# Performance work log

Hardware: AMD Instinct MI355X
Metric: run time of the kernel (lower is better)

Reference implementation:

```python
import jax, jax.numpy as jnp
import numpy as np

# Workspace layout (static slice bounds, per init_kwargs)
SS, SE = 0, 512        # spoke
HPS, HPE = 512, 768    # hub private
HSS, HSE = 768, 1024   # hub shared
TS, TE = 1024, 1088    # tag
HS, HE = 512, 1024     # full hub (priv + shared) for the read path

B, T, D_STATE, D_MODEL, D_LATENT = 8, 4096, 1088, 1024, 128


def setup_inputs() -> dict:
    key = jax.random.key(0)
    ks = jax.random.split(key, 10)
    scale = 0.02  # typical init scale for learned projections
    return {
        "S": jax.random.normal(ks[0], (B, T, D_STATE), jnp.float32),
        "w_spoke": jax.random.normal(ks[1], (B, T, SE - SS), jnp.float32),
        "w_hub_priv": jax.random.normal(ks[2], (B, T, HPE - HPS), jnp.float32),
        "w_hub_shared": jax.random.normal(ks[3], (B, T, HSE - HSS), jnp.float32),
        "tag": jax.random.normal(ks[4], (B, T, TE - TS), jnp.float32),
        "W_read": jax.random.normal(ks[5], (D_MODEL, D_STATE), jnp.float32) * scale,
        "cache": jnp.zeros((B, T, D_LATENT), jnp.float32),
        "latent": jax.random.normal(ks[6], (B, T, D_LATENT), jnp.float32),
        "Wk": jax.random.normal(ks[7], (D_MODEL, D_LATENT), jnp.float32) * scale,
        "Wv": jax.random.normal(ks[8], (D_MODEL, D_LATENT), jnp.float32) * scale,
    }


def reference(S, w_spoke, w_hub_priv, w_hub_shared, tag, W_read, cache, latent, Wk, Wv):
    # --- fused_workspace_write: four independent slice-adds into S ---
    S = S.at[:, :, SS:SE].add(w_spoke)
    S = S.at[:, :, HPS:HPE].add(w_hub_priv)
    S = S.at[:, :, HSS:HSE].add(w_hub_shared)
    S = S.at[:, :, TS:TE].add(tag)

    # --- fused_workspace_read: concat(spoke, hub, tag) then F.linear(., W_read) ---
    readable = jnp.concatenate(
        [S[:, :, SS:SE], S[:, :, HS:HE], S[:, :, TS:TE]], axis=-1
    )  # (B, T, D_STATE)
    out = jnp.einsum("btr,dr->btd", readable, W_read)  # (B, T, D_MODEL)

    # --- CWTLatentCache.update: overwrite latents at start_position=0 ---
    cache = jax.lax.dynamic_update_slice(cache, latent, (0, 0, 0))

    # --- K/V reconstruction from compressed latents via up-projections ---
    k = jnp.einsum("btl,dl->btd", cache, Wk)  # (B, T, D_MODEL)
    v = jnp.einsum("btl,dl->btd", cache, Wv)  # (B, T, D_MODEL)
    return (out, k, v)
```

## Files before the change

### kernel.cpp

```cpp
#include <hip/hip_runtime.h>

typedef __attribute__((ext_vector_type(8))) _Float16 half8;
typedef __attribute__((ext_vector_type(2))) __fp16 half2r;
typedef __attribute__((ext_vector_type(4))) float f32x4;

#define AS1 __attribute__((address_space(1)))
#define AS3 __attribute__((address_space(3)))

union H2U { half2r h; unsigned int u; };
union Frag { half8 v; unsigned long long d[2]; };

__device__ __forceinline__ unsigned int pk(float a, float b) {
    H2U x; x.h = __builtin_amdgcn_cvt_pkrtz(a, b); return x.u;
}

__device__ __forceinline__ void gload_lds16(const void* g, void* l) {
    __builtin_amdgcn_global_load_lds((const AS1 unsigned int*)g,
                                     (AS3 unsigned int*)l, 16, 0, 0);
}

#define W1_ROWB 2176
#define WS2_OFF 2228224
#define W2_ROWB 256
#define A_ROWB  2176

__device__ __forceinline__ void pick_w(int ks, const float* wsp, const float* whp,
                                       const float* whs, const float* wtg,
                                       const float*& wbase, int& wstr, int& wko) {
    if (ks < 8)       { wbase = wsp; wstr = 512; wko = ks * 64; }
    else if (ks < 12) { wbase = whp; wstr = 256; wko = ks * 64 - 512; }
    else if (ks < 16) { wbase = whs; wstr = 256; wko = ks * 64 - 768; }
    else              { wbase = wtg; wstr = 64;  wko = 0; }
}

__global__ __launch_bounds__(256) void prep_w(const float* __restrict__ Wr,
                                              const float* __restrict__ Wk,
                                              const float* __restrict__ Wv,
                                              char* __restrict__ ws) {
    int id = blockIdx.x * 256 + threadIdx.x;
    if (id < 272 * 1024) {
        int n = id / 272;
        int k = (id % 272) * 4;
        f32x4 w = *(const f32x4*)(Wr + (size_t)n * 1088 + k);
        uint2 q; q.x = pk(w.x, w.y); q.y = pk(w.z, w.w);
        size_t off = (size_t)n * W1_ROWB + ((k >> 6) << 7)
                   + (((k & 63) << 1) ^ ((n & 7) << 4));
        *(uint2*)(ws + off) = q;
    } else {
        int j = id - 272 * 1024;
        int r = j >> 5;
        int k = (j & 31) << 2;
        const float* src = (r < 1024) ? (Wk + (size_t)r * 128 + k)
                                      : (Wv + (size_t)(r - 1024) * 128 + k);
        f32x4 w = *(const f32x4*)src;
        uint2 q; q.x = pk(w.x, w.y); q.y = pk(w.z, w.w);
        size_t off = WS2_OFF + (size_t)r * W2_ROWB + ((k >> 6) << 7)
                   + (((k & 63) << 1) ^ ((r & 7) << 4));
        *(uint2*)(ws + off) = q;
    }
}

__global__ __launch_bounds__(256)
void fuse_a(const float* __restrict__ S, const float* __restrict__ wsp,
            const float* __restrict__ whp, const float* __restrict__ whs,
            const float* __restrict__ wtg, char* __restrict__ a16) {
    int u = blockIdx.x * 256 + threadIdx.x;
    int row = u / 272;
    int rem = u % 272;
    int ks = rem >> 4;
    int k4 = (rem & 15) << 2;

    const float* wbase; int wstr, wko;
    pick_w(ks, wsp, whp, whs, wtg, wbase, wstr, wko);

    f32x4 s4 = *(const f32x4*)(S + (size_t)row * 1088 + ks * 64 + k4);
    f32x4 w4 = *(const f32x4*)(wbase + (size_t)row * wstr + wko + k4);
    uint2 q; q.x = pk(s4.x + w4.x, s4.y + w4.y);
             q.y = pk(s4.z + w4.z, s4.w + w4.w);
    size_t off = (size_t)row * A_ROWB + (ks << 7)
               + (((k4) << 1) ^ ((row & 7) << 4));
    *(uint2*)(a16 + off) = q;
}

__global__ __launch_bounds__(256, 2)
void gemm_read(const char* __restrict__ wsA, const char* __restrict__ wws,
               float* __restrict__ out) {
    __shared__ char lds[65536];

    int bid = blockIdx.x;
    int wg   = (bid & 7) * 256 + (bid >> 3);
    int mblk = wg >> 3, nblk = wg & 7;
    int m0 = mblk << 7, n0 = nblk << 7;

    int tid = threadIdx.x;
    int lane = tid & 63, wid = tid >> 6;
    int wm = (wid >> 1) << 6, wn = (wid & 1) << 6;
    int lp = lane & 15, lg = lane >> 4;

    f32x4 acc[4][4] = {};

#define STAGE_T(KS, DL, BASE, ROWB, R0) do {                              \
        const char* grow = (BASE) + (size_t)(R0) * (ROWB) + (KS) * 128;   \
        _Pragma("unroll")                                                 \
        for (int c = 0; c < 4; ++c) {                                     \
            int s = c * 4096 + wid * 1024 + lane * 16;                    \
            int rr = s >> 7, cb = s & 127;                                \
            gload_lds16(grow + (size_t)rr * (ROWB) + cb,                  \
                        (DL) + c * 4096 + wid * 1024);                    \
        }                                                                 \
    } while (0)

#define COMPUTE(AL, BL) do {                                              \
        _Pragma("unroll")                                                 \
        for (int b = 0; b < 2; ++b) {                                     \
            Frag af[4], bf[4];                                            \
            _Pragma("unroll")                                             \
            for (int f = 0; f < 4; ++f) {                                 \
                int ra = wm + f * 16 + lp;  int xa = (ra & 7) << 4;       \
                af[f].d[0] = *(const unsigned long long*)((AL) + (ra << 7) + ((b * 64 + lg * 8) ^ xa));      \
                af[f].d[1] = *(const unsigned long long*)((AL) + (ra << 7) + ((b * 64 + 32 + lg * 8) ^ xa)); \
                int rb = wn + f * 16 + lp;  int xb = (rb & 7) << 4;       \
                bf[f].d[0] = *(const unsigned long long*)((BL) + (rb << 7) + ((b * 64 + lg * 8) ^ xb));      \
                bf[f].d[1] = *(const unsigned long long*)((BL) + (rb << 7) + ((b * 64 + 32 + lg * 8) ^ xb)); \
            }                                                             \
            _Pragma("unroll")                                             \
            for (int i = 0; i < 4; ++i)                                   \
                _Pragma("unroll")                                         \
                for (int j = 0; j < 4; ++j)                               \
                    acc[i][j] = __builtin_amdgcn_mfma_f32_16x16x32_f16(af[i].v, bf[j].v, acc[i][j], 0, 0, 0); \
        }                                                                 \
    } while (0)

    STAGE_T(0, lds,         wsA, A_ROWB,  m0);
    STAGE_T(0, lds + 32768, wws, W1_ROWB, n0);
    __syncthreads();

    for (int ks = 0; ks < 17; ++ks) {
        int co = (ks & 1) ? 16384 : 0;
        int no = co ^ 16384;
        if (ks < 16) {
            STAGE_T(ks + 1, lds + no,         wsA, A_ROWB,  m0);
            STAGE_T(ks + 1, lds + 32768 + no, wws, W1_ROWB, n0);
        }
        COMPUTE(lds + co, lds + 32768 + co);
        __syncthreads();
    }

    #pragma unroll
    for (int i = 0; i < 4; ++i)
        #pragma unroll
        for (int j = 0; j < 4; ++j) {
            int row = m0 + wm + i * 16 + (lg << 2);
            int col = n0 + wn + j * 16 + lp;
            float* p = out + (size_t)row * 1024 + col;
            #pragma unroll
            for (int r = 0; r < 4; ++r) p[(size_t)r * 1024] = acc[i][j][r];
        }
#undef STAGE_T
#undef COMPUTE
}

__global__ __launch_bounds__(256, 2)
void gemm_kv(const float* __restrict__ lat, const char* __restrict__ ws2,
             float* __restrict__ outk, float* __restrict__ outv) {
    __shared__ char lds[32768];
    char* Al = lds;
    char* Bl = lds + 16384;

    int bid = blockIdx.x;
    int wg   = (bid & 7) * 512 + (bid >> 3);
    int mblk = wg >> 4, nb = wg & 15;
    int m0 = mblk << 7;
    int nrow0 = nb << 7;
    float* out = (nb < 8) ? outk : outv;
    int n0 = (nb & 7) << 7;

    int tid = threadIdx.x;
    int lane = tid & 63, wid = tid >> 6;
    int wm = (wid >> 1) << 6, wn = (wid & 1) << 6;
    int lp = lane & 15, lg = lane >> 4;

    f32x4 acc[4][4] = {};

    for (int ks = 0; ks < 2; ++ks) {
        __syncthreads();
        {
            const char* wrow = ws2 + (size_t)nrow0 * W2_ROWB + ks * 128;
            #pragma unroll
            for (int c = 0; c < 4; ++c) {
                int s = c * 4096 + wid * 1024 + lane * 16;
                int n = s >> 7, cb = s & 127;
                gload_lds16(wrow + (size_t)n * W2_ROWB + cb,
                            Bl + c * 4096 + wid * 1024);
            }
        }
        #pragma unroll
        for (int i = 0; i < 8; ++i) {
            int u = i * 256 + tid;
            int row = u >> 4;
            int k4 = (u & 15) << 2;
            f32x4 s4 = *(const f32x4*)(lat + (size_t)(m0 + row) * 128 + ks * 64 + k4);
            uint2 q; q.x = pk(s4.x, s4.y); q.y = pk(s4.z, s4.w);
            *(uint2*)(Al + (row << 7) + ((k4 << 1) ^ ((row & 7) << 4))) = q;
        }
        __syncthreads();

        #pragma unroll
        for (int b = 0; b < 2; ++b) {
            Frag af[4], bf[4];
            #pragma unroll
            for (int f = 0; f < 4; ++f) {
                int ra = wm + f * 16 + lp;  int xa = (ra & 7) << 4;
                af[f].d[0] = *(const unsigned long long*)(Al + (ra << 7) + ((b * 64 + lg * 8) ^ xa));
                af[f].d[1] = *(const unsigned long long*)(Al + (ra << 7) + ((b * 64 + 32 + lg * 8) ^ xa));
                int rb = wn + f * 16 + lp;  int xb = (rb & 7) << 4;
                bf[f].d[0] = *(const unsigned long long*)(Bl + (rb << 7) + ((b * 64 + lg * 8) ^ xb));
                bf[f].d[1] = *(const unsigned long long*)(Bl + (rb << 7) + ((b * 64 + 32 + lg * 8) ^ xb));
            }
            #pragma unroll
            for (int i = 0; i < 4; ++i)
                #pragma unroll
                for (int j = 0; j < 4; ++j)
                    acc[i][j] = __builtin_amdgcn_mfma_f32_16x16x32_f16(af[i].v, bf[j].v, acc[i][j], 0, 0, 0);
        }
    }

    #pragma unroll
    for (int i = 0; i < 4; ++i)
        #pragma unroll
        for (int j = 0; j < 4; ++j) {
            int row = m0 + wm + i * 16 + (lg << 2);
            int col = n0 + wn + j * 16 + lp;
            float* p = out + (size_t)row * 1024 + col;
            #pragma unroll
            for (int r = 0; r < 4; ++r) p[(size_t)r * 1024] = acc[i][j][r];
        }
}

extern "C" void kernel_launch(void* const* d_in, const int* in_sizes, int n_in,
                              void* d_out, int out_size, void* d_ws, size_t ws_size,
                              hipStream_t stream) {
    const float* S   = (const float*)d_in[0];
    const float* wsp = (const float*)d_in[1];
    const float* whp = (const float*)d_in[2];
    const float* whs = (const float*)d_in[3];
    const float* wtg = (const float*)d_in[4];
    const float* Wr  = (const float*)d_in[5];
    const float* lat = (const float*)d_in[7];
    const float* Wk  = (const float*)d_in[8];
    const float* Wv  = (const float*)d_in[9];
    float* out = (float*)d_out;
    char*  ws  = (char*)d_ws;

    char* a16 = (char*)(out + 67108864ull);

    hipLaunchKernelGGL(prep_w, dim3(1344), dim3(256), 0, stream, Wr, Wk, Wv, ws);
    hipLaunchKernelGGL(fuse_a, dim3(34816), dim3(256), 0, stream,
                       S, wsp, whp, whs, wtg, a16);
    hipLaunchKernelGGL(gemm_read, dim3(2048), dim3(256), 0, stream,
                       a16, ws, out);
    hipLaunchKernelGGL(gemm_kv, dim3(4096), dim3(256), 0, stream,
                       lat, ws + WS2_OFF, out + 33554432ull, out + 67108864ull);
}
```

Measured before the change: 269.4 us.

## Merge prep/fuse kernels and interleave read and KV GEMMs in one launch

Combines the weight-conversion and activation fuse kernels into one launch. It then merges the read GEMM and the K/V GEMMs into a single kernel whose blocks are interleaved, so the compute-heavy read tiles and the memory-heavy KV tiles share the GPU at the same time. When the workspace is large enough, the fp16 A buffer moves there so all GEMMs can run together. Otherwise it falls back to a read+K kernel followed by a V kernel. This removes launch gaps and tail effects, at the cost of higher LDS use for the KV tiles (64KB allocated) and more branching.

```diff
diff --git a/kernel.cpp b/kernel.cpp
--- a/kernel.cpp
+++ b/kernel.cpp
@@ -23,6 +23,8 @@
 #define WS2_OFF 2228224
 #define W2_ROWB 256
 #define A_ROWB  2176
+#define WS2_SZ  524288
+#define A16_SZ  71303168ull
 
 __device__ __forceinline__ void pick_w(int ks, const float* wsp, const float* whp,
                                        const float* whs, const float* wtg,
@@ -33,62 +35,60 @@
     else              { wbase = wtg; wstr = 64;  wko = 0; }
 }
 
-__global__ __launch_bounds__(256) void prep_w(const float* __restrict__ Wr,
-                                              const float* __restrict__ Wk,
-                                              const float* __restrict__ Wv,
-                                              char* __restrict__ ws) {
-    int id = blockIdx.x * 256 + threadIdx.x;
-    if (id < 272 * 1024) {
-        int n = id / 272;
-        int k = (id % 272) * 4;
-        f32x4 w = *(const f32x4*)(Wr + (size_t)n * 1088 + k);
-        uint2 q; q.x = pk(w.x, w.y); q.y = pk(w.z, w.w);
-        size_t off = (size_t)n * W1_ROWB + ((k >> 6) << 7)
-                   + (((k & 63) << 1) ^ ((n & 7) << 4));
-        *(uint2*)(ws + off) = q;
+__global__ __launch_bounds__(256)
+void prep_fuse(const float* __restrict__ S, const float* __restrict__ wsp,
+               const float* __restrict__ whp, const float* __restrict__ whs,
+               const float* __restrict__ wtg, char* __restrict__ a16,
+               const float* __restrict__ Wr, const float* __restrict__ Wk,
+               const float* __restrict__ Wv, char* __restrict__ ws) {
+    int bid = blockIdx.x;
+    int tid = threadIdx.x;
+    if (bid < 34816) {
+        int u = bid * 256 + tid;
+        int row = u / 272;
+        int rem = u % 272;
+        int ks = rem >> 4;
+        int k4 = (rem & 15) << 2;
+
+        const float* wbase; int wstr, wko;
+        pick_w(ks, wsp, whp, whs, wtg, wbase, wstr, wko);
+
+        f32x4 s4 = *(const f32x4*)(S + (size_t)row * 1088 + ks * 64 + k4);
+        f32x4 w4 = *(const f32x4*)(wbase + (size_t)row * wstr + wko + k4);
+        uint2 q; q.x = pk(s4.x + w4.x, s4.y + w4.y);
+                 q.y = pk(s4.z + w4.z, s4.w + w4.w);
+        size_t off = (size_t)row * A_ROWB + (ks << 7)
+                   + (((k4) << 1) ^ ((row & 7) << 4));
+        *(uint2*)(a16 + off) = q;
     } else {
-        int j = id - 272 * 1024;
-        int r = j >> 5;
-        int k = (j & 31) << 2;
-        const float* src = (r < 1024) ? (Wk + (size_t)r * 128 + k)
-                                      : (Wv + (size_t)(r - 1024) * 128 + k);
-        f32x4 w = *(const f32x4*)src;
-        uint2 q; q.x = pk(w.x, w.y); q.y = pk(w.z, w.w);
-        size_t off = WS2_OFF + (size_t)r * W2_ROWB + ((k >> 6) << 7)
-                   + (((k & 63) << 1) ^ ((r & 7) << 4));
-        *(uint2*)(ws + off) = q;
+        int id = (bid - 34816) * 256 + tid;
+        if (id < 272 * 1024) {
+            int n = id / 272;
+            int k = (id % 272) * 4;
+            f32x4 w = *(const f32x4*)(Wr + (size_t)n * 1088 + k);
+            uint2 q; q.x = pk(w.x, w.y); q.y = pk(w.z, w.w);
+            size_t off = (size_t)n * W1_ROWB + ((k >> 6) << 7)
+                       + (((k & 63) << 1) ^ ((n & 7) << 4));
+            *(uint2*)(ws + off) = q;
+        } else {
+            int j = id - 272 * 1024;
+            int r = j >> 5;
+            int k = (j & 31) << 2;
+            const float* src = (r < 1024) ? (Wk + (size_t)r * 128 + k)
+                                          : (Wv + (size_t)(r - 1024) * 128 + k);
+            f32x4 w = *(const f32x4*)src;
+            uint2 q; q.x = pk(w.x, w.y); q.y = pk(w.z, w.w);
+            size_t off = WS2_OFF + (size_t)r * W2_ROWB + ((k >> 6) << 7)
+                       + (((k & 63) << 1) ^ ((r & 7) << 4));
+            *(uint2*)(ws + off) = q;
+        }
     }
 }
 
-__global__ __launch_bounds__(256)
-void fuse_a(const float* __restrict__ S, const float* __restrict__ wsp,
-            const float* __restrict__ whp, const float* __restrict__ whs,
-            const float* __restrict__ wtg, char* __restrict__ a16) {
-    int u = blockIdx.x * 256 + threadIdx.x;
-    int row = u / 272;
-    int rem = u % 272;
-    int ks = rem >> 4;
-    int k4 = (rem & 15) << 2;
-
-    const float* wbase; int wstr, wko;
-    pick_w(ks, wsp, whp, whs, wtg, wbase, wstr, wko);
-
-    f32x4 s4 = *(const f32x4*)(S + (size_t)row * 1088 + ks * 64 + k4);
-    f32x4 w4 = *(const f32x4*)(wbase + (size_t)row * wstr + wko + k4);
-    uint2 q; q.x = pk(s4.x + w4.x, s4.y + w4.y);
-             q.y = pk(s4.z + w4.z, s4.w + w4.w);
-    size_t off = (size_t)row * A_ROWB + (ks << 7)
-               + (((k4) << 1) ^ ((row & 7) << 4));
-    *(uint2*)(a16 + off) = q;
-}
-
-__global__ __launch_bounds__(256, 2)
-void gemm_read(const char* __restrict__ wsA, const char* __restrict__ wws,
-               float* __restrict__ out) {
-    __shared__ char lds[65536];
-
-    int bid = blockIdx.x;
-    int wg   = (bid & 7) * 256 + (bid >> 3);
+__device__ __forceinline__
+void body_read(int idx, const char* __restrict__ wsA, const char* __restrict__ wws,
+               float* __restrict__ out, char* lds) {
+    int wg   = (idx & 7) * 256 + (idx >> 3);
     int mblk = wg >> 3, nblk = wg & 7;
     int m0 = mblk << 7, n0 = nblk << 7;
 
@@ -160,16 +160,15 @@
 #undef COMPUTE
 }
 
-__global__ __launch_bounds__(256, 2)
-void gemm_kv(const float* __restrict__ lat, const char* __restrict__ ws2,
-             float* __restrict__ outk, float* __restrict__ outv) {
-    __shared__ char lds[32768];
+__device__ __forceinline__
+void body_kv(int idx, int nkv8, int nb_shift, int nb_mask, int nb_off,
+             const float* __restrict__ lat, const char* __restrict__ ws2,
+             float* __restrict__ outk, float* __restrict__ outv, char* lds) {
     char* Al = lds;
     char* Bl = lds + 16384;
 
-    int bid = blockIdx.x;
-    int wg   = (bid & 7) * 512 + (bid >> 3);
-    int mblk = wg >> 4, nb = wg & 15;
+    int wg   = (idx & 7) * nkv8 + (idx >> 3);
+    int mblk = wg >> nb_shift, nb = nb_off + (wg & nb_mask);
     int m0 = mblk << 7;
     int nrow0 = nb << 7;
     float* out = (nb < 8) ? outk : outv;
@@ -235,6 +234,41 @@
             #pragma unroll
             for (int r = 0; r < 4; ++r) p[(size_t)r * 1024] = acc[i][j][r];
         }
+}
+
+__global__ __launch_bounds__(256, 2)
+void gemm_all(const char* __restrict__ wsA, const char* __restrict__ wws,
+              float* __restrict__ out, const float* __restrict__ lat,
+              const char* __restrict__ ws2,
+              float* __restrict__ outk, float* __restrict__ outv) {
+    __shared__ char lds[65536];
+    int bid = blockIdx.x;
+    int g = bid >> 3, o = bid & 7;
+    int gq = g / 3, gm = g % 3;
+    if (gm == 0)
+        body_read(gq * 8 + o, wsA, wws, out, lds);
+    else
+        body_kv((gq * 2 + (gm - 1)) * 8 + o, 512, 4, 15, 0, lat, ws2, outk, outv, lds);
+}
+
+__global__ __launch_bounds__(256, 2)
+void gemm_rk(const char* __restrict__ wsA, const char* __restrict__ wws,
+             float* __restrict__ out, const float* __restrict__ lat,
+             const char* __restrict__ ws2, float* __restrict__ outk) {
+    __shared__ char lds[65536];
+    int bid = blockIdx.x;
+    int g = bid >> 3, o = bid & 7;
+    if ((g & 1) == 0)
+        body_read((g >> 1) * 8 + o, wsA, wws, out, lds);
+    else
+        body_kv((g >> 1) * 8 + o, 256, 3, 7, 0, lat, ws2, outk, outk, lds);
+}
+
+__global__ __launch_bounds__(256, 2)
+void gemm_v(const float* __restrict__ lat, const char* __restrict__ ws2,
+            float* __restrict__ outk, float* __restrict__ outv) {
+    __shared__ char lds[32768];
+    body_kv(blockIdx.x, 256, 3, 7, 8, lat, ws2, outk, outv, lds);
 }
 
 extern "C" void kernel_launch(void* const* d_in, const int* in_sizes, int n_in,
@@ -252,13 +286,25 @@
     float* out = (float*)d_out;
     char*  ws  = (char*)d_ws;
 
-    char* a16 = (char*)(out + 67108864ull);
-
-    hipLaunchKernelGGL(prep_w, dim3(1344), dim3(256), 0, stream, Wr, Wk, Wv, ws);
-    hipLaunchKernelGGL(fuse_a, dim3(34816), dim3(256), 0, stream,
-                       S, wsp, whp, whs, wtg, a16);
-    hipLaunchKernelGGL(gemm_read, dim3(2048), dim3(256), 0, stream,
-                       a16, ws, out);
-    hipLaunchKernelGGL(gemm_kv, dim3(4096), dim3(256), 0, stream,
-                       lat, ws + WS2_OFF, out + 33554432ull, out + 67108864ull);
-}
+    float* outk = out + 33554432ull;
+    float* outv = out + 67108864ull;
+
+    const size_t A16_WS_OFF = (size_t)WS2_OFF + WS2_SZ;
+    const size_t ws_need = A16_WS_OFF + A16_SZ;
+
+    if (ws_size >= ws_need) {
+        char* a16 = ws + A16_WS_OFF;
+        hipLaunchKernelGGL(prep_fuse, dim3(36160), dim3(256), 0, stream,
+                           S, wsp, whp, whs, wtg, a16, Wr, Wk, Wv, ws);
+        hipLaunchKernelGGL(gemm_all, dim3(6144), dim3(256), 0, stream,
+                           a16, ws, out, lat, ws + WS2_OFF, outk, outv);
+    } else {
+        char* a16 = (char*)outv;
+        hipLaunchKernelGGL(prep_fuse, dim3(36160), dim3(256), 0, stream,
+                           S, wsp, whp, whs, wtg, a16, Wr, Wk, Wv, ws);
+        hipLaunchKernelGGL(gemm_rk, dim3(4096), dim3(256), 0, stream,
+                           a16, ws, out, lat, ws + WS2_OFF, outk);
+        hipLaunchKernelGGL(gemm_v, dim3(2048), dim3(256), 0, stream,
+                           lat, ws + WS2_OFF, outk, outv);
+    }
+}
```

Result: slower. 279.8 us (+3.8%).

## Fuse workspace slice-add and fp16 conversion into read GEMM A-tile loading

Applied to the files above, without the earlier changes.

Removes the separate fuse_a pass, which materialised an fp16 copy of S+w in global memory. The read GEMM now loads fp32 S and the matching write slices into registers, adds and packs them to fp16, and stores the swizzled A tile into LDS while the previous tile is being computed. This avoids a full extra read/write pass over the large activation tensors. The cost is that each N-block re-reads fp32 A data, and the extra registers may hurt occupancy.

```diff
diff --git a/kernel.cpp b/kernel.cpp
--- a/kernel.cpp
+++ b/kernel.cpp
@@ -22,7 +22,6 @@
 #define W1_ROWB 2176
 #define WS2_OFF 2228224
 #define W2_ROWB 256
-#define A_ROWB  2176
 
 __device__ __forceinline__ void pick_w(int ks, const float* wsp, const float* whp,
                                        const float* whs, const float* wtg,
@@ -60,31 +59,11 @@
     }
 }
 
-__global__ __launch_bounds__(256)
-void fuse_a(const float* __restrict__ S, const float* __restrict__ wsp,
-            const float* __restrict__ whp, const float* __restrict__ whs,
-            const float* __restrict__ wtg, char* __restrict__ a16) {
-    int u = blockIdx.x * 256 + threadIdx.x;
-    int row = u / 272;
-    int rem = u % 272;
-    int ks = rem >> 4;
-    int k4 = (rem & 15) << 2;
-
-    const float* wbase; int wstr, wko;
-    pick_w(ks, wsp, whp, whs, wtg, wbase, wstr, wko);
-
-    f32x4 s4 = *(const f32x4*)(S + (size_t)row * 1088 + ks * 64 + k4);
-    f32x4 w4 = *(const f32x4*)(wbase + (size_t)row * wstr + wko + k4);
-    uint2 q; q.x = pk(s4.x + w4.x, s4.y + w4.y);
-             q.y = pk(s4.z + w4.z, s4.w + w4.w);
-    size_t off = (size_t)row * A_ROWB + (ks << 7)
-               + (((k4) << 1) ^ ((row & 7) << 4));
-    *(uint2*)(a16 + off) = q;
-}
-
 __global__ __launch_bounds__(256, 2)
-void gemm_read(const char* __restrict__ wsA, const char* __restrict__ wws,
-               float* __restrict__ out) {
+void gemm_read_f(const float* __restrict__ S, const float* __restrict__ wsp,
+                 const float* __restrict__ whp, const float* __restrict__ whs,
+                 const float* __restrict__ wtg, const char* __restrict__ wws,
+                 float* __restrict__ out) {
     __shared__ char lds[65536];
 
     int bid = blockIdx.x;
@@ -98,51 +77,81 @@
     int lp = lane & 15, lg = lane >> 4;
 
     f32x4 acc[4][4] = {};
-
-#define STAGE_T(KS, DL, BASE, ROWB, R0) do {                              \
-        const char* grow = (BASE) + (size_t)(R0) * (ROWB) + (KS) * 128;   \
-        _Pragma("unroll")                                                 \
-        for (int c = 0; c < 4; ++c) {                                     \
-            int s = c * 4096 + wid * 1024 + lane * 16;                    \
-            int rr = s >> 7, cb = s & 127;                                \
-            gload_lds16(grow + (size_t)rr * (ROWB) + cb,                  \
-                        (DL) + c * 4096 + wid * 1024);                    \
-        }                                                                 \
-    } while (0)
-
-#define COMPUTE(AL, BL) do {                                              \
-        _Pragma("unroll")                                                 \
-        for (int b = 0; b < 2; ++b) {                                     \
-            Frag af[4], bf[4];                                            \
-            _Pragma("unroll")                                             \
-            for (int f = 0; f < 4; ++f) {                                 \
-                int ra = wm + f * 16 + lp;  int xa = (ra & 7) << 4;       \
+    f32x4 sreg[8], wreg[8];
+
+#define LOAD_A(KS) do {                                                       \
+        const float* wbase; int wstr, wko;                                    \
+        pick_w((KS), wsp, whp, whs, wtg, wbase, wstr, wko);                   \
+        _Pragma("unroll")                                                     \
+        for (int c = 0; c < 8; ++c) {                                         \
+            int u = c * 256 + tid;                                            \
+            int row = u >> 4;                                                 \
+            int k4 = (u & 15) << 2;                                           \
+            sreg[c] = *(const f32x4*)(S + (size_t)(m0 + row) * 1088           \
+                                        + (KS) * 64 + k4);                    \
+            wreg[c] = *(const f32x4*)(wbase + (size_t)(m0 + row) * wstr       \
+                                        + wko + k4);                          \
+        }                                                                     \
+    } while (0)
+
+#define WRITE_A(DL) do {                                                      \
+        _Pragma("unroll")                                                     \
+        for (int c = 0; c < 8; ++c) {                                         \
+            int u = c * 256 + tid;                                            \
+            int row = u >> 4;                                                 \
+            int k4 = (u & 15) << 2;                                           \
+            uint2 q; q.x = pk(sreg[c].x + wreg[c].x, sreg[c].y + wreg[c].y);  \
+                     q.y = pk(sreg[c].z + wreg[c].z, sreg[c].w + wreg[c].w);  \
+            *(uint2*)((DL) + (row << 7) + ((k4 << 1) ^ ((row & 7) << 4))) = q;\
+        }                                                                     \
+    } while (0)
+
+#define STAGE_B(KS, DL) do {                                                  \
+        const char* grow = wws + (size_t)n0 * W1_ROWB + (KS) * 128;           \
+        _Pragma("unroll")                                                     \
+        for (int c = 0; c < 4; ++c) {                                         \
+            int s = c * 4096 + wid * 1024 + lane * 16;                        \
+            int rr = s >> 7, cb = s & 127;                                    \
+            gload_lds16(grow + (size_t)rr * W1_ROWB + cb,                     \
+                        (DL) + c * 4096 + wid * 1024);                        \
+        }                                                                     \
+    } while (0)
+
+#define COMPUTE(AL, BL) do {                                                  \
+        _Pragma("unroll")                                                     \
+        for (int b = 0; b < 2; ++b) {                                         \
+            Frag af[4], bf[4];                                                \
+            _Pragma("unroll")                                                 \
+            for (int f = 0; f < 4; ++f) {                                     \
+                int ra = wm + f * 16 + lp;  int xa = (ra & 7) << 4;           \
                 af[f].d[0] = *(const unsigned long long*)((AL) + (ra << 7) + ((b * 64 + lg * 8) ^ xa));      \
                 af[f].d[1] = *(const unsigned long long*)((AL) + (ra << 7) + ((b * 64 + 32 + lg * 8) ^ xa)); \
-                int rb = wn + f * 16 + lp;  int xb = (rb & 7) << 4;       \
+                int rb = wn + f * 16 + lp;  int xb = (rb & 7) << 4;           \
                 bf[f].d[0] = *(const unsigned long long*)((BL) + (rb << 7) + ((b * 64 + lg * 8) ^ xb));      \
                 bf[f].d[1] = *(const unsigned long long*)((BL) + (rb << 7) + ((b * 64 + 32 + lg * 8) ^ xb)); \
-            }                                                             \
-            _Pragma("unroll")                                             \
-            for (int i = 0; i < 4; ++i)                                   \
-                _Pragma("unroll")                                         \
-                for (int j = 0; j < 4; ++j)                               \
+            }                                                                 \
+            _Pragma("unroll")                                                 \
+            for (int i = 0; i < 4; ++i)                                       \
+                _Pragma("unroll")                                             \
+                for (int j = 0; j < 4; ++j)                                   \
                     acc[i][j] = __builtin_amdgcn_mfma_f32_16x16x32_f16(af[i].v, bf[j].v, acc[i][j], 0, 0, 0); \
-        }                                                                 \
-    } while (0)
-
-    STAGE_T(0, lds,         wsA, A_ROWB,  m0);
-    STAGE_T(0, lds + 32768, wws, W1_ROWB, n0);
+        }                                                                     \
+    } while (0)
+
+    LOAD_A(0);
+    STAGE_B(0, lds + 32768);
+    WRITE_A(lds);
     __syncthreads();
 
     for (int ks = 0; ks < 17; ++ks) {
         int co = (ks & 1) ? 16384 : 0;
         int no = co ^ 16384;
         if (ks < 16) {
-            STAGE_T(ks + 1, lds + no,         wsA, A_ROWB,  m0);
-            STAGE_T(ks + 1, lds + 32768 + no, wws, W1_ROWB, n0);
+            LOAD_A(ks + 1);
+            STAGE_B(ks + 1, lds + 32768 + no);
         }
         COMPUTE(lds + co, lds + 32768 + co);
+        if (ks < 16) WRITE_A(lds + no);
         __syncthreads();
     }
 
@@ -156,7 +165,9 @@
             #pragma unroll
             for (int r = 0; r < 4; ++r) p[(size_t)r * 1024] = acc[i][j][r];
         }
-#undef STAGE_T
+#undef LOAD_A
+#undef WRITE_A
+#undef STAGE_B
 #undef COMPUTE
 }
 
@@ -252,13 +263,12 @@
     float* out = (float*)d_out;
     char*  ws  = (char*)d_ws;
 
-    char* a16 = (char*)(out + 67108864ull);
+    float* outk = out + 33554432ull;
+    float* outv = out + 67108864ull;
 
     hipLaunchKernelGGL(prep_w, dim3(1344), dim3(256), 0, stream, Wr, Wk, Wv, ws);
-    hipLaunchKernelGGL(fuse_a, dim3(34816), dim3(256), 0, stream,
-                       S, wsp, whp, whs, wtg, a16);
-    hipLaunchKernelGGL(gemm_read, dim3(2048), dim3(256), 0, stream,
-                       a16, ws, out);
+    hipLaunchKernelGGL(gemm_read_f, dim3(2048), dim3(256), 0, stream,
+                       S, wsp, whp, whs, wtg, ws, out);
     hipLaunchKernelGGL(gemm_kv, dim3(4096), dim3(256), 0, stream,
-                       lat, ws + WS2_OFF, out + 33554432ull, out + 67108864ull);
-}
+                       lat, ws + WS2_OFF, outk, outv);
+}
```

Result: slower. 317.0 us (+17.7%).

## Halve gemm_read K-step to 32 to shrink LDS and raise occupancy

Applied to the files above, without the earlier changes.

The read GEMM now stages 32-wide K tiles (64 bytes per row) instead of 64-wide, which halves its LDS footprint to 32 KB and raises the launch-bounds occupancy hint from 2 to 4 blocks. The fp16 A and W layouts written by fuse_a and prep_w are re-swizzled to match, using 64-byte segments with an 8-byte XOR swizzle. The aim is more resident waves to hide global-load latency. In exchange the loop runs twice as many iterations with twice as many barriers, and the register budget per thread is tighter.

```diff
diff --git a/kernel.cpp b/kernel.cpp
--- a/kernel.cpp
+++ b/kernel.cpp
@@ -43,8 +43,8 @@
         int k = (id % 272) * 4;
         f32x4 w = *(const f32x4*)(Wr + (size_t)n * 1088 + k);
         uint2 q; q.x = pk(w.x, w.y); q.y = pk(w.z, w.w);
-        size_t off = (size_t)n * W1_ROWB + ((k >> 6) << 7)
-                   + (((k & 63) << 1) ^ ((n & 7) << 4));
+        size_t off = (size_t)n * W1_ROWB + ((k >> 5) << 6)
+                   + ((((k >> 2) & 7) ^ (n & 7)) << 3);
         *(uint2*)(ws + off) = q;
     } else {
         int j = id - 272 * 1024;
@@ -77,15 +77,16 @@
     f32x4 w4 = *(const f32x4*)(wbase + (size_t)row * wstr + wko + k4);
     uint2 q; q.x = pk(s4.x + w4.x, s4.y + w4.y);
              q.y = pk(s4.z + w4.z, s4.w + w4.w);
-    size_t off = (size_t)row * A_ROWB + (ks << 7)
-               + (((k4) << 1) ^ ((row & 7) << 4));
+    int kk = ks * 64 + k4;
+    size_t off = (size_t)row * A_ROWB + ((kk >> 5) << 6)
+               + ((((kk >> 2) & 7) ^ (row & 7)) << 3);
     *(uint2*)(a16 + off) = q;
 }
 
-__global__ __launch_bounds__(256, 2)
+__global__ __launch_bounds__(256, 4)
 void gemm_read(const char* __restrict__ wsA, const char* __restrict__ wws,
                float* __restrict__ out) {
-    __shared__ char lds[65536];
+    __shared__ char lds[32768];
 
     int bid = blockIdx.x;
     int wg   = (bid & 7) * 256 + (bid >> 3);
@@ -99,50 +100,47 @@
 
     f32x4 acc[4][4] = {};
 
-#define STAGE_T(KS, DL, BASE, ROWB, R0) do {                              \
-        const char* grow = (BASE) + (size_t)(R0) * (ROWB) + (KS) * 128;   \
+#define STAGE32(T, DL, BASE, ROWB, R0) do {                               \
+        const char* grow = (BASE) + (size_t)(R0) * (ROWB) + (T) * 64;     \
         _Pragma("unroll")                                                 \
-        for (int c = 0; c < 4; ++c) {                                     \
+        for (int c = 0; c < 2; ++c) {                                     \
             int s = c * 4096 + wid * 1024 + lane * 16;                    \
-            int rr = s >> 7, cb = s & 127;                                \
+            int rr = s >> 6, cb = s & 63;                                 \
             gload_lds16(grow + (size_t)rr * (ROWB) + cb,                  \
                         (DL) + c * 4096 + wid * 1024);                    \
         }                                                                 \
     } while (0)
 
-#define COMPUTE(AL, BL) do {                                              \
+#define COMPUTE32(AL, BL) do {                                            \
+        Frag af[4], bf[4];                                                \
         _Pragma("unroll")                                                 \
-        for (int b = 0; b < 2; ++b) {                                     \
-            Frag af[4], bf[4];                                            \
+        for (int f = 0; f < 4; ++f) {                                     \
+            int ra = wm + f * 16 + lp;  int xa = ra & 7;                  \
+            af[f].d[0] = *(const unsigned long long*)((AL) + (ra << 6) + ((lg ^ xa) << 3));        \
+            af[f].d[1] = *(const unsigned long long*)((AL) + (ra << 6) + (((4 + lg) ^ xa) << 3));  \
+            int rb = wn + f * 16 + lp;  int xb = rb & 7;                  \
+            bf[f].d[0] = *(const unsigned long long*)((BL) + (rb << 6) + ((lg ^ xb) << 3));        \
+            bf[f].d[1] = *(const unsigned long long*)((BL) + (rb << 6) + (((4 + lg) ^ xb) << 3));  \
+        }                                                                 \
+        _Pragma("unroll")                                                 \
+        for (int i = 0; i < 4; ++i)                                       \
             _Pragma("unroll")                                             \
-            for (int f = 0; f < 4; ++f) {                                 \
-                int ra = wm + f * 16 + lp;  int xa = (ra & 7) << 4;       \
-                af[f].d[0] = *(const unsigned long long*)((AL) + (ra << 7) + ((b * 64 + lg * 8) ^ xa));      \
-                af[f].d[1] = *(const unsigned long long*)((AL) + (ra << 7) + ((b * 64 + 32 + lg * 8) ^ xa)); \
-                int rb = wn + f * 16 + lp;  int xb = (rb & 7) << 4;       \
-                bf[f].d[0] = *(const unsigned long long*)((BL) + (rb << 7) + ((b * 64 + lg * 8) ^ xb));      \
-                bf[f].d[1] = *(const unsigned long long*)((BL) + (rb << 7) + ((b * 64 + 32 + lg * 8) ^ xb)); \
-            }                                                             \
-            _Pragma("unroll")                                             \
-            for (int i = 0; i < 4; ++i)                                   \
-                _Pragma("unroll")                                         \
-                for (int j = 0; j < 4; ++j)                               \
-                    acc[i][j] = __builtin_amdgcn_mfma_f32_16x16x32_f16(af[i].v, bf[j].v, acc[i][j], 0, 0, 0); \
-        }                                                                 \
+            for (int j = 0; j < 4; ++j)                                   \
+                acc[i][j] = __builtin_amdgcn_mfma_f32_16x16x32_f16(af[i].v, bf[j].v, acc[i][j], 0, 0, 0); \
     } while (0)
 
-    STAGE_T(0, lds,         wsA, A_ROWB,  m0);
-    STAGE_T(0, lds + 32768, wws, W1_ROWB, n0);
+    STAGE32(0, lds,         wsA, A_ROWB,  m0);
+    STAGE32(0, lds + 16384, wws, W1_ROWB, n0);
     __syncthreads();
 
-    for (int ks = 0; ks < 17; ++ks) {
-        int co = (ks & 1) ? 16384 : 0;
-        int no = co ^ 16384;
-        if (ks < 16) {
-            STAGE_T(ks + 1, lds + no,         wsA, A_ROWB,  m0);
-            STAGE_T(ks + 1, lds + 32768 + no, wws, W1_ROWB, n0);
-        }
-        COMPUTE(lds + co, lds + 32768 + co);
+    for (int t = 0; t < 34; ++t) {
+        int co = (t & 1) ? 8192 : 0;
+        int no = co ^ 8192;
+        if (t < 33) {
+            STAGE32(t + 1, lds + no,         wsA, A_ROWB,  m0);
+            STAGE32(t + 1, lds + 16384 + no, wws, W1_ROWB, n0);
+        }
+        COMPUTE32(lds + co, lds + 16384 + co);
         __syncthreads();
     }
 
@@ -156,8 +154,8 @@
             #pragma unroll
             for (int r = 0; r < 4; ++r) p[(size_t)r * 1024] = acc[i][j][r];
         }
-#undef STAGE_T
-#undef COMPUTE
+#undef STAGE32
+#undef COMPUTE32
 }
 
 __global__ __launch_bounds__(256, 2)
```

Result: no change. 270.7 us (+0.5%).
